# Kernel optimization log

Hardware: AMD Instinct MI355X
Metric: run time of the kernel (lower is better)

The kernel has to match this reference:

```python
import jax, jax.numpy as jnp
import numpy as np

EPS = 1e-12


def setup_inputs() -> dict:
    key = jax.random.key(0)
    k = jax.random.split(key, 6)
    B, C, T, A = 8, 1536, 4096, 128
    x = jax.random.normal(k[0], (B, C, T), dtype=jnp.float32)
    lengths = jax.random.randint(k[1], (B,), T // 2, T + 1, dtype=jnp.int64)
    W1 = jax.random.normal(k[2], (A, 3 * C), dtype=jnp.float32) * (1.0 / np.sqrt(3 * C))
    b1 = jax.random.normal(k[3], (A,), dtype=jnp.float32) * 0.01
    W2 = jax.random.normal(k[4], (1, A), dtype=jnp.float32) * (1.0 / np.sqrt(A))
    b2 = jax.random.normal(k[5], (1,), dtype=jnp.float32) * 0.01
    return {"x": x, "lengths": lengths, "W1": W1, "b1": b1, "W2": W2, "b2": b2}


def reference(x, lengths, W1, b1, W2, b2):
    # x: [B, C, T]
    B, C, T = x.shape
    mask = (jnp.arange(T)[None, :] < lengths[:, None]).astype(x.dtype)  # [B, T]
    m3 = mask[:, None, :]  # [B, 1, T]

    # causal (cumulative) mean / std for global context
    count = jnp.clip(jnp.cumsum(mask, axis=1), 1.0)[:, None, :]        # [B, 1, T]
    causal_mean = jnp.cumsum(x * m3, axis=2) / count                   # [B, C, T]
    causal_var = jnp.cumsum(x * x * m3, axis=2) / count - causal_mean ** 2
    causal_std = jnp.sqrt(jnp.clip(causal_var, EPS))

    attn_in = jnp.concatenate([x, causal_mean, causal_std], axis=1)    # [B, 3C, T]
    attn_in = attn_in.transpose(0, 2, 1)                               # [B, T, 3C]

    h = jnp.tanh(attn_in @ W1.T + b1)                                  # [B, T, A]
    logits = (h @ W2.T + b2)[..., 0]                                   # [B, T]

    # logits are query-independent, so causal softmax row q is
    # exp(l_k) / cumsum(exp(l))_q for k <= q -> O(T*C) prefix scan.
    e = jnp.exp(logits - jnp.max(logits, axis=1, keepdims=True))       # [B, T]
    Z = jnp.cumsum(e, axis=1)[:, None, :]                              # [B, 1, T]
    ew = e[:, None, :]                                                 # [B, 1, T]

    weighted_mean = jnp.cumsum(ew * x, axis=2) / Z                     # [B, C, T]
    sq_diff = (x - weighted_mean) ** 2
    weighted_var = jnp.cumsum(ew * sq_diff, axis=2) / Z
    weighted_std = jnp.sqrt(jnp.clip(weighted_var, EPS))

    # each causal softmax row sums to 1 -> final weights are 1/(T+eps)
    fw = 1.0 / (jnp.asarray(T, x.dtype) + EPS)
    final_mean = jnp.sum(weighted_mean, axis=2) * fw                   # [B, C]
    final_std = jnp.sum(weighted_std, axis=2) * fw
    return jnp.concatenate([final_mean, final_std], axis=1)            # [B, 2C]
```

## Files before the change

kernel.cpp:

```cpp
#include <hip/hip_runtime.h>
#include <hip/hip_bf16.h>

#define B_ 8
#define C_ 1536
#define T_ 4096
#define A_ 128
#define K3_ 4608
#define M32_ 128
#define SCW_ 104

typedef _Float16 h8  __attribute__((ext_vector_type(8)));
typedef float    f4  __attribute__((ext_vector_type(4)));

__global__ void k0_pack(const float* __restrict__ W1, _Float16* __restrict__ W1f) {
    int i = blockIdx.x * 256 + threadIdx.x;
    if (i >= A_ * K3_) return;
    int a = i / K3_, k = i - a * K3_;
    int t8 = a >> 4, r15 = a & 15;
    int kb = k >> 5, q = (k >> 3) & 3, j = k & 7;
    int lane = q * 16 + r15;
    W1f[(size_t)((kb * 8 + t8) * 64 + lane) * 8 + j] = (_Float16)W1[i];
}

__global__ __launch_bounds__(256) void k1_carry(
    const float* __restrict__ x, const int* __restrict__ lens,
    float2* __restrict__ carry)
{
    const int rowid = blockIdx.x * 4 + (threadIdx.x >> 6);
    const int lane  = threadIdx.x & 63;
    const int b     = rowid / C_;
    const int len   = lens[b];
    const float* xr = x + (size_t)rowid * T_;
    float2* cp = carry + (size_t)rowid * M32_;
    const int grp = lane >> 3;
    float base1 = 0.f, base2 = 0.f;
#pragma unroll
    for (int g = 0; g < 16; ++g) {
        const int t0g = g * 256;
        if (t0g >= len) {
            if ((lane & 7) == 0) cp[g * 8 + grp] = make_float2(base1, base2);
            continue;
        }
        float4 v = *(const float4*)(xr + t0g + lane * 4);
        float s1, s2;
        if (t0g + 256 <= len) {
            s1 = v.x + v.y + v.z + v.w;
            s2 = v.x * v.x + v.y * v.y + v.z * v.z + v.w * v.w;
        } else {
            const int tb = t0g + lane * 4;
            float vs[4] = {v.x, v.y, v.z, v.w};
            s1 = 0.f; s2 = 0.f;
#pragma unroll
            for (int j = 0; j < 4; ++j) {
                float m = (tb + j < len) ? vs[j] : 0.f;
                s1 += m; s2 += m * vs[j];
            }
        }
        float g1 = s1, g2 = s2;
        g1 += __shfl_xor(g1, 1, 64); g2 += __shfl_xor(g2, 1, 64);
        g1 += __shfl_xor(g1, 2, 64); g2 += __shfl_xor(g2, 2, 64);
        g1 += __shfl_xor(g1, 4, 64); g2 += __shfl_xor(g2, 4, 64);
        float V1 = g1, V2 = g2;
#pragma unroll
        for (int d = 8; d < 64; d <<= 1) {
            float o1 = __shfl_up(V1, d, 64);
            float o2 = __shfl_up(V2, d, 64);
            if (lane >= d) { V1 += o1; V2 += o2; }
        }
        const float e1 = V1 - g1, e2 = V2 - g2;
        if ((lane & 7) == 0) cp[g * 8 + grp] = make_float2(base1 + e1, base2 + e2);
        base1 += __shfl(V1, 63, 64);
        base2 += __shfl(V2, 63, 64);
    }
}

__global__ __launch_bounds__(256) void k1b_T(
    const float2* __restrict__ carry, float2* __restrict__ carryT)
{
    __shared__ float2 t[64][65];
    const int bid = blockIdx.x;
    const int b = bid / 48;
    const int r = bid - b * 48;
    const int ct = r >> 1, mt = r & 1;
    const int c0 = ct * 64, m0 = mt * 64;
    const int tx = threadIdx.x & 63, ty = threadIdx.x >> 6;
#pragma unroll
    for (int i = 0; i < 16; ++i) {
        int cl = i * 4 + ty;
        t[cl][tx] = carry[((size_t)(b * C_ + c0 + cl)) * M32_ + m0 + tx];
    }
    __syncthreads();
#pragma unroll
    for (int i = 0; i < 16; ++i) {
        int ml = i * 4 + ty;
        carryT[((size_t)b * M32_ + m0 + ml) * C_ + c0 + tx] = t[tx][ml];
    }
}

__global__ __launch_bounds__(256, 2) void k2f(
    const float* __restrict__ x, const int* __restrict__ lens,
    const float2* __restrict__ carryT, const _Float16* __restrict__ W1f,
    const float* __restrict__ b1, const float* __restrict__ W2,
    float* __restrict__ logits)
{
    __shared__ __align__(16) char smem[32768];
    __shared__ float s_b1[A_], s_w2[A_];

    const int tid = threadIdx.x, lane = tid & 63, w = tid >> 6;
    const int s   = w & 1;
    const int tch = w >> 1;
    const int bid = blockIdx.x;
    const int b   = bid >> 6;
    const int m   = ((bid & 63) << 1) + tch;
    const int t0  = m << 5;
    const int len = lens[b];
    if (tid < A_) { s_b1[tid] = b1[tid]; s_w2[tid] = W2[tid]; }

    const int kc = lane >> 1;
    const int th = lane & 1;
    const int c_base = s * 768;
    _Float16* sc = (_Float16*)smem + w * (32 * SCW_);
    const h8* W1f8 = (const h8*)W1f;
    const bool full = (t0 + 32) <= len;
    const int tb = t0 + th * 16;

    f4 acc[2][8] = {};

    const float* xptr = x + ((size_t)b * C_ + c_base + kc) * T_ + tb;
    float4 xv0 = ((const float4*)xptr)[0];
    float4 xv1 = ((const float4*)xptr)[1];
    float4 xv2 = ((const float4*)xptr)[2];
    float4 xv3 = ((const float4*)xptr)[3];

    for (int step = 0; step < 24; ++step) {
        float xs[16];
        *(float4*)&xs[0]  = xv0; *(float4*)&xs[4]  = xv1;
        *(float4*)&xs[8]  = xv2; *(float4*)&xs[12] = xv3;
        if (step < 23) {
            xptr += 32 * (size_t)T_;
            xv0 = ((const float4*)xptr)[0];
            xv1 = ((const float4*)xptr)[1];
            xv2 = ((const float4*)xptr)[2];
            xv3 = ((const float4*)xptr)[3];
        }
        const float2 cr =
            carryT[((size_t)b * M32_ + m) * C_ + c_base + step * 32 + kc];

        float ls1 = 0.f, ls2 = 0.f;
        if (full) {
#pragma unroll
            for (int j = 0; j < 16; ++j) { ls1 += xs[j]; ls2 += xs[j] * xs[j]; }
        } else {
#pragma unroll
            for (int j = 0; j < 16; ++j) {
                float mv = (tb + j < len) ? xs[j] : 0.f;
                ls1 += mv; ls2 += mv * xs[j];
            }
        }
        const float o1 = __shfl_xor(ls1, 1, 64);
        const float o2 = __shfl_xor(ls2, 1, 64);
        float r1 = cr.x + (th ? o1 : 0.f);
        float r2 = cr.y + (th ? o2 : 0.f);
#pragma unroll
        for (int j = 0; j < 16; ++j) {
            const float xval = xs[j];
            const float mv = (full || (tb + j < len)) ? xval : 0.f;
            r1 += mv; r2 += mv * xval;
            const float rn = __builtin_amdgcn_rcpf((float)min(tb + j + 1, len));
            const float mn = r1 * rn;
            const float var = r2 * rn - mn * mn;
            const float sd = sqrtf(fmaxf(var, 1e-12f));
            const int row = th * 16 + j;
            sc[row * SCW_ + kc]      = (_Float16)xval;
            sc[row * SCW_ + 32 + kc] = (_Float16)mn;
            sc[row * SCW_ + 64 + kc] = (_Float16)sd;
        }
        const int t15 = lane & 15, k8 = lane >> 4;
        const int kbS = s * 24 + step;
#pragma unroll
        for (int p = 0; p < 3; ++p) {
            h8 bf0 = *(const h8*)&sc[t15 * SCW_ + p * 32 + k8 * 8];
            h8 bf1 = *(const h8*)&sc[(16 + t15) * SCW_ + p * 32 + k8 * 8];
            const int kb = p * 48 + kbS;
#pragma unroll
            for (int ii = 0; ii < 8; ++ii) {
                h8 af = W1f8[(size_t)(kb * 8 + ii) * 64 + lane];
                acc[0][ii] = __builtin_amdgcn_mfma_f32_16x16x32_f16(af, bf0, acc[0][ii], 0, 0, 0);
                acc[1][ii] = __builtin_amdgcn_mfma_f32_16x16x32_f16(af, bf1, acc[1][ii], 0, 0, 0);
            }
        }
    }

    __syncthreads();
    float* red_f = (float*)smem;
    if (s == 1) {
        float* r = red_f + tch * 4096;
#pragma unroll
        for (int nn = 0; nn < 2; ++nn)
#pragma unroll
            for (int ii = 0; ii < 8; ++ii)
#pragma unroll
                for (int rg = 0; rg < 4; ++rg)
                    r[(nn * 32 + ii * 4 + rg) * 64 + lane] = acc[nn][ii][rg];
    }
    __syncthreads();
    if (s == 0) {
        float* r = red_f + tch * 4096;
        const int q = lane >> 4;
#pragma unroll
        for (int nn = 0; nn < 2; ++nn) {
            float pr = 0.f;
#pragma unroll
            for (int ii = 0; ii < 8; ++ii)
#pragma unroll
                for (int rg = 0; rg < 4; ++rg) {
                    float v = acc[nn][ii][rg] + r[(nn * 32 + ii * 4 + rg) * 64 + lane];
                    int a = ii * 16 + q * 4 + rg;
                    pr += tanhf(v + s_b1[a]) * s_w2[a];
                }
            pr += __shfl_xor(pr, 16, 64);
            pr += __shfl_xor(pr, 32, 64);
            if (lane < 16)
                logits[(size_t)b * T_ + t0 + nn * 16 + lane] = pr;
        }
    }
}

__global__ __launch_bounds__(1024) void k3_softmax(
    const float* __restrict__ logits, float* __restrict__ earr,
    float* __restrict__ zarr)
{
    __shared__ float wsum[16];
    const int b = blockIdx.x, tid = threadIdx.x, lane = tid & 63, w = tid >> 6;
    float4 v = *(const float4*)(logits + (size_t)b * T_ + tid * 4);
    float e0 = expf(v.x), e1 = expf(v.y), e2 = expf(v.z), e3 = expf(v.w);
    float s = (e0 + e1) + (e2 + e3);
    float V = s;
#pragma unroll
    for (int d = 1; d < 64; d <<= 1) {
        float o = __shfl_up(V, d, 64);
        if (lane >= d) V += o;
    }
    if (lane == 63) wsum[w] = V;
    __syncthreads();
    float wb = 0.f;
#pragma unroll
    for (int i = 0; i < 16; ++i) wb += (i < w) ? wsum[i] : 0.f;
    float run = wb + (V - s);
    float4 ev, zv;
    ev.x = e0; run += e0; zv.x = run;
    ev.y = e1; run += e1; zv.y = run;
    ev.z = e2; run += e2; zv.z = run;
    ev.w = e3; run += e3; zv.w = run;
    *(float4*)(earr + (size_t)b * T_ + tid * 4) = ev;
    *(float4*)(zarr + (size_t)b * T_ + tid * 4) = zv;
}

__global__ __launch_bounds__(256) void k4_wstats(
    const float* __restrict__ x, const float* __restrict__ earr,
    const float* __restrict__ zarr, float* __restrict__ out)
{
    const int rowid = blockIdx.x * 4 + (threadIdx.x >> 6);
    const int lane  = threadIdx.x & 63;
    const int b = rowid / C_;
    const int c = rowid - b * C_;
    const float* xr = x + (size_t)rowid * T_;
    const float* er = earr + (size_t)b * T_;
    const float* zr = zarr + (size_t)b * T_;
    float am = 0.f, asd = 0.f;
    float baseS = 0.f, baseD = 0.f;
#pragma unroll
    for (int g = 0; g < 16; ++g) {
        const int off = g * 256 + lane * 4;
        float4 xv = *(const float4*)(xr + off);
        float4 ev = *(const float4*)(er + off);
        float4 zv = *(const float4*)(zr + off);
        float s0 = ev.x * xv.x;
        float s1 = s0 + ev.y * xv.y;
        float s2 = s1 + ev.z * xv.z;
        float s3 = s2 + ev.w * xv.w;
        float V = s3;
#pragma unroll
        for (int d = 1; d < 64; d <<= 1) {
            float o = __shfl_up(V, d, 64);
            if (lane >= d) V += o;
        }
        const float Sx = baseS + (V - s3);
        baseS += __shfl(V, 63, 64);
        const float rz0 = __builtin_amdgcn_rcpf(zv.x);
        const float rz1 = __builtin_amdgcn_rcpf(zv.y);
        const float rz2 = __builtin_amdgcn_rcpf(zv.z);
        const float rz3 = __builtin_amdgcn_rcpf(zv.w);
        const float wm0 = (Sx + s0) * rz0;
        const float wm1 = (Sx + s1) * rz1;
        const float wm2 = (Sx + s2) * rz2;
        const float wm3 = (Sx + s3) * rz3;
        am += (wm0 + wm1) + (wm2 + wm3);
        const float d0 = xv.x - wm0;
        const float d1 = xv.y - wm1;
        const float d2 = xv.z - wm2;
        const float d3 = xv.w - wm3;
        float q0 = ev.x * d0 * d0;
        float q1 = q0 + ev.y * d1 * d1;
        float q2 = q1 + ev.z * d2 * d2;
        float q3 = q2 + ev.w * d3 * d3;
        float W = q3;
#pragma unroll
        for (int d = 1; d < 64; d <<= 1) {
            float o = __shfl_up(W, d, 64);
            if (lane >= d) W += o;
        }
        const float Dx = baseD + (W - q3);
        baseD += __shfl(W, 63, 64);
        const float v0 = (Dx + q0) * rz0;
        const float v1 = (Dx + q1) * rz1;
        const float v2 = (Dx + q2) * rz2;
        const float v3 = (Dx + q3) * rz3;
        asd += (sqrtf(fmaxf(v0, 1e-12f)) + sqrtf(fmaxf(v1, 1e-12f)))
             + (sqrtf(fmaxf(v2, 1e-12f)) + sqrtf(fmaxf(v3, 1e-12f)));
    }
#pragma unroll
    for (int d = 1; d < 64; d <<= 1) {
        am  += __shfl_xor(am, d, 64);
        asd += __shfl_xor(asd, d, 64);
    }
    if (lane == 0) {
        out[(size_t)b * (2 * C_) + c]      = am  * (1.f / 4096.f);
        out[(size_t)b * (2 * C_) + C_ + c] = asd * (1.f / 4096.f);
    }
}

extern "C" void kernel_launch(void* const* d_in, const int* in_sizes, int n_in,
                              void* d_out, int out_size, void* d_ws, size_t ws_size,
                              hipStream_t stream) {
    const float* x    = (const float*)d_in[0];
    const int*   lens = (const int*)d_in[1];
    const float* W1   = (const float*)d_in[2];
    const float* b1   = (const float*)d_in[3];
    const float* W2   = (const float*)d_in[4];
    float* out = (float*)d_out;
    char* ws = (char*)d_ws;

    float2*    carry  = (float2*)ws;
    float2*    carryT = (float2*)(ws + 12582912);
    _Float16*  W1f    = (_Float16*)(ws + 25165824);
    float*     logits = (float*)(ws + 26345472);
    float*     earr   = (float*)(ws + 26476544);
    float*     zarr   = (float*)(ws + 26607616);

    k0_pack   <<<(A_ * K3_ + 255) / 256, 256, 0, stream>>>(W1, W1f);
    k1_carry  <<<(B_ * C_) / 4, 256, 0, stream>>>(x, lens, carry);
    k1b_T     <<<B_ * 48, 256, 0, stream>>>(carry, carryT);
    k2f       <<<B_ * 64, 256, 0, stream>>>(x, lens, carryT, W1f, b1, W2, logits);
    k3_softmax<<<B_, 1024, 0, stream>>>(logits, earr, zarr);
    k4_wstats <<<(B_ * C_) / 4, 256, 0, stream>>>(x, earr, zarr, out);
}
```

Baseline: 470.9 us.

## Split k2 channel reduction across four waves per time chunk

Each block of the fused stats+GEMM kernel now handles a single 32-step time chunk, with the four waves splitting the channel dimension into quarters instead of two chunks times two halves. This doubles the grid size and raises the launch-bounds occupancy target, and a two-stage LDS reduction combines the partial accumulators. The aim is better latency hiding and load balance. The costs are extra reduction syncs and possible register pressure or spills under the tighter launch bound.

```diff
diff --git a/kernel.cpp b/kernel.cpp
--- a/kernel.cpp
+++ b/kernel.cpp
@@ -97,7 +97,7 @@
     }
 }
 
-__global__ __launch_bounds__(256, 2) void k2f(
+__global__ __launch_bounds__(256, 4) void k2g(
     const float* __restrict__ x, const int* __restrict__ lens,
     const float2* __restrict__ carryT, const _Float16* __restrict__ W1f,
     const float* __restrict__ b1, const float* __restrict__ W2,
@@ -107,18 +107,16 @@
     __shared__ float s_b1[A_], s_w2[A_];
 
     const int tid = threadIdx.x, lane = tid & 63, w = tid >> 6;
-    const int s   = w & 1;
-    const int tch = w >> 1;
     const int bid = blockIdx.x;
-    const int b   = bid >> 6;
-    const int m   = ((bid & 63) << 1) + tch;
+    const int b   = bid >> 7;
+    const int m   = bid & 127;
     const int t0  = m << 5;
     const int len = lens[b];
     if (tid < A_) { s_b1[tid] = b1[tid]; s_w2[tid] = W2[tid]; }
 
     const int kc = lane >> 1;
     const int th = lane & 1;
-    const int c_base = s * 768;
+    const int c_base = w * 384;
     _Float16* sc = (_Float16*)smem + w * (32 * SCW_);
     const h8* W1f8 = (const h8*)W1f;
     const bool full = (t0 + 32) <= len;
@@ -132,11 +130,11 @@
     float4 xv2 = ((const float4*)xptr)[2];
     float4 xv3 = ((const float4*)xptr)[3];
 
-    for (int step = 0; step < 24; ++step) {
+    for (int step = 0; step < 12; ++step) {
         float xs[16];
         *(float4*)&xs[0]  = xv0; *(float4*)&xs[4]  = xv1;
         *(float4*)&xs[8]  = xv2; *(float4*)&xs[12] = xv3;
-        if (step < 23) {
+        if (step < 11) {
             xptr += 32 * (size_t)T_;
             xv0 = ((const float4*)xptr)[0];
             xv1 = ((const float4*)xptr)[1];
@@ -176,7 +174,7 @@
             sc[row * SCW_ + 64 + kc] = (_Float16)sd;
         }
         const int t15 = lane & 15, k8 = lane >> 4;
-        const int kbS = s * 24 + step;
+        const int kbS = w * 12 + step;
 #pragma unroll
         for (int p = 0; p < 3; ++p) {
             h8 bf0 = *(const h8*)&sc[t15 * SCW_ + p * 32 + k8 * 8];
@@ -192,9 +190,9 @@
     }
 
     __syncthreads();
-    float* red_f = (float*)smem;
-    if (s == 1) {
-        float* r = red_f + tch * 4096;
+    float* red = (float*)smem;
+    if (w >= 2) {
+        float* r = red + (size_t)(w - 2) * 4096;
 #pragma unroll
         for (int nn = 0; nn < 2; ++nn)
 #pragma unroll
@@ -204,8 +202,28 @@
                     r[(nn * 32 + ii * 4 + rg) * 64 + lane] = acc[nn][ii][rg];
     }
     __syncthreads();
-    if (s == 0) {
-        float* r = red_f + tch * 4096;
+    if (w < 2) {
+        float* r = red + (size_t)w * 4096;
+#pragma unroll
+        for (int nn = 0; nn < 2; ++nn)
+#pragma unroll
+            for (int ii = 0; ii < 8; ++ii)
+#pragma unroll
+                for (int rg = 0; rg < 4; ++rg)
+                    acc[nn][ii][rg] += r[(nn * 32 + ii * 4 + rg) * 64 + lane];
+    }
+    __syncthreads();
+    if (w == 1) {
+#pragma unroll
+        for (int nn = 0; nn < 2; ++nn)
+#pragma unroll
+            for (int ii = 0; ii < 8; ++ii)
+#pragma unroll
+                for (int rg = 0; rg < 4; ++rg)
+                    red[(nn * 32 + ii * 4 + rg) * 64 + lane] = acc[nn][ii][rg];
+    }
+    __syncthreads();
+    if (w == 0) {
         const int q = lane >> 4;
 #pragma unroll
         for (int nn = 0; nn < 2; ++nn) {
@@ -214,7 +232,7 @@
             for (int ii = 0; ii < 8; ++ii)
 #pragma unroll
                 for (int rg = 0; rg < 4; ++rg) {
-                    float v = acc[nn][ii][rg] + r[(nn * 32 + ii * 4 + rg) * 64 + lane];
+                    float v = acc[nn][ii][rg] + red[(nn * 32 + ii * 4 + rg) * 64 + lane];
                     int a = ii * 16 + q * 4 + rg;
                     pr += tanhf(v + s_b1[a]) * s_w2[a];
                 }
@@ -351,7 +369,7 @@
     k0_pack   <<<(A_ * K3_ + 255) / 256, 256, 0, stream>>>(W1, W1f);
     k1_carry  <<<(B_ * C_) / 4, 256, 0, stream>>>(x, lens, carry);
     k1b_T     <<<B_ * 48, 256, 0, stream>>>(carry, carryT);
-    k2f       <<<B_ * 64, 256, 0, stream>>>(x, lens, carryT, W1f, b1, W2, logits);
+    k2g       <<<B_ * M32_, 256, 0, stream>>>(x, lens, carryT, W1f, b1, W2, logits);
     k3_softmax<<<B_, 1024, 0, stream>>>(logits, earr, zarr);
     k4_wstats <<<(B_ * C_) / 4, 256, 0, stream>>>(x, earr, zarr, out);
 }
```

Measured after the change: 600.1 us. 1.27x slower.
